# Kernel optimization log

Measured on AMD Instinct MI355X. Metric: run time of the kernel, lower is better.

The kernel has to match this reference:

```python
import jax, jax.numpy as jnp
import numpy as np

N = 64        # n_nodes per graph
H = 128       # hidden channels (128x0e + 128x1o)
NB = 8        # radial bessel basis size
L = 2         # num_interactions
R_MAX = 5.0
AVG_NEIGH = 63.0
DIM = 3       # output vector dim
B = 64        # batch (vmapped)
T = 32        # time-embedding dim
S = 5         # num_species


def _edges(n):
    # fully-connected graph, no self loops (static shapes, jit-friendly)
    s, r = np.meshgrid(np.arange(n), np.arange(n), indexing='ij')
    m = s != r
    return jnp.asarray(s[m]), jnp.asarray(r[m])


def setup_inputs() -> dict:
    key = jax.random.key(0)
    ks = jax.random.split(key, 12)
    sc = 0.05
    return {
        'positions': jax.random.normal(ks[0], (B, N, 3), jnp.float32),
        'node_features': jax.random.randint(ks[1], (B, N), 0, S).astype(jnp.int64),
        'global_features': jax.random.normal(ks[2], (B, T), jnp.float32),
        'emb': jax.random.normal(ks[3], (S, H), jnp.float32) * sc,
        'Wt': jax.random.normal(ks[4], (T, H), jnp.float32) * sc,
        'Wr1': jax.random.normal(ks[5], (L, NB, H), jnp.float32) * sc,
        'Wr2': jax.random.normal(ks[6], (L, H, H), jnp.float32) * sc,
        'Wupd': jax.random.normal(ks[7], (L, H, H), jnp.float32) * sc,
        'Wmix': jax.random.normal(ks[8], (L, H, H), jnp.float32) * sc,
        'Wg1': jax.random.normal(ks[9], (H, H), jnp.float32) * sc,
        'Wg2': jax.random.normal(ks[10], (H, H), jnp.float32) * sc,
        'final_scaling': jnp.ones((), jnp.float32),
    }


def _call_single(pos, z, t, emb, Wt, Wr1, Wr2, Wupd, Wmix, Wg1, Wg2, final_scaling):
    snd, rcv = _edges(N)
    ev = pos[rcv] - pos[snd]                               # [E,3] edge vectors (gather)
    r = jnp.sqrt(jnp.sum(ev * ev, axis=-1) + 1e-12)        # [E]
    u = ev / r[:, None]                                    # unit directions
    # Bessel radial basis with cosine cutoff (r_max acts as soft radius graph)
    n = jnp.arange(1, NB + 1, dtype=pos.dtype)
    rb = jnp.sin(n * jnp.pi * r[:, None] / R_MAX) / r[:, None]   # [E,NB]
    fc = 0.5 * (jnp.cos(jnp.pi * r / R_MAX) + 1.0) * (r < R_MAX)
    rb = rb * fc[:, None]
    # node embedding from species + time embedding
    h = emb[z] + t @ Wt                                    # [N,H] scalar features
    v = jnp.zeros((N, H, DIM), pos.dtype)                  # vector (1o) features
    for l in range(L):
        w = jax.nn.silu(rb @ Wr1[l]) @ Wr2[l]              # [E,H] radial weights
        m0 = w * h[snd]                                    # [E,H] scalar messages
        m1 = m0[:, :, None] * u[:, None, :]                # [E,H,3] vector messages
        a0 = jax.ops.segment_sum(m0, rcv, num_segments=N) / AVG_NEIGH
        a1 = jax.ops.segment_sum(m1, rcv, num_segments=N) / AVG_NEIGH
        h = h + a0 @ Wupd[l]
        v = v + jnp.einsum('ngd,gh->nhd', a1, Wmix[l])
    # equivariant readout: scalar gate per channel contracts vector channels
    g = jax.nn.silu(h @ Wg1) @ Wg2                         # [N,H]
    out = jnp.einsum('nhd,nh->nd', v, g)                   # [N,3]
    return out * final_scaling


def reference(positions, node_features, global_features, emb, Wt, Wr1, Wr2, Wupd, Wmix, Wg1, Wg2, final_scaling):
    f = lambda p, z, t: _call_single(p, z, t, emb, Wt, Wr1, Wr2, Wupd, Wmix, Wg1, Wg2, final_scaling)
    return jax.vmap(f)(positions, node_features, global_features)
```

## Files before the change

### kernel.cpp

```cpp
#include <hip/hip_runtime.h>
#include <math.h>

#define NN 64
#define HH 128
#define NBB 8
#define TT 32
#define BB 64
#define NROW (BB * NN)
#define PLANE ((size_t)NROW * HH)
#define WR1OFF (8 * 16384)

typedef __attribute__((ext_vector_type(8))) short short8;
typedef __attribute__((ext_vector_type(4))) float f32x4;
typedef __attribute__((ext_vector_type(2))) float f32x2;
typedef __attribute__((ext_vector_type(2))) unsigned int u32x2;

__device__ __forceinline__ float silu_f(float x) {
  return x * __builtin_amdgcn_rcpf(1.0f + __expf(-x));
}

__device__ __forceinline__ unsigned short bf1(float x) {
  __bf16 h = (__bf16)x;
  return *(unsigned short*)&h;
}
__device__ __forceinline__ unsigned bf2(float lo, float hi) {
  return (unsigned)bf1(lo) | ((unsigned)bf1(hi) << 16);
}

__device__ __forceinline__ void gemm8(
    const unsigned short (*sA)[136], const unsigned short* __restrict__ Bp,
    int w, int nlo, int quad, f32x4 C[2]) {
  const short8 z8 = {0, 0, 0, 0, 0, 0, 0, 0};
  short8 afr[4];
#pragma unroll
  for (int kt = 0; kt < 4; ++kt)
    afr[kt] = (nlo < 8) ? *(const short8*)&sA[nlo][kt * 32 + quad * 8] : z8;
#pragma unroll
  for (int nt = 0; nt < 2; ++nt)
#pragma unroll
    for (int kt = 0; kt < 4; ++kt) {
      short8 bfr = *(const short8*)&Bp[((kt * 128 + w * 32 + nt * 16 + nlo) * 4 + quad) * 8];
      C[nt] = __builtin_amdgcn_mfma_f32_16x16x32_bf16(afr[kt], bfr, C[nt], 0, 0, 0);
    }
}

__global__ __launch_bounds__(256) void k_init(
    const float* __restrict__ emb, const int* __restrict__ z,
    const float* __restrict__ gf, const float* __restrict__ Wt,
    const float* __restrict__ Wr1, const float* __restrict__ Wr2,
    const float* __restrict__ Wupd, const float* __restrict__ Wmix,
    const float* __restrict__ Wg1, const float* __restrict__ Wg2,
    float* __restrict__ h, unsigned short* __restrict__ Wpack) {
  __shared__ float tvec[HH];
  __shared__ int sz[NN];
  int b4 = blockIdx.x, tid = threadIdx.x;
#pragma unroll
  for (int ii = 0; ii < 2; ++ii) {
    int idx = b4 * 512 + ii * 256 + tid;
    int m = idx >> 14;
    int local = idx & 16383;
    float val;
    if (m < 2) val = Wr2[idx];
    else if (m < 4) val = Wupd[idx - 32768];
    else if (m < 6) val = Wmix[idx - 65536];
    else if (m == 6) val = Wg1[local];
    else val = Wg2[local];
    int k = local >> 7, n = local & 127;
    int kt = k >> 5, q = (k >> 3) & 3, j = k & 7;
    Wpack[(idx & ~16383) + (((kt * 128 + n) * 4 + q) * 8) + j] = bf1(val);
  }
  if (tid < 32) {
    int e = b4 * 32 + tid;
    int l = e >> 12, p = e & 4095;
    int n = p >> 5, q = (p >> 3) & 3, j = p & 7;
    float val = (q == 0) ? Wr1[l * NBB * HH + j * HH + n] : 0.f;
    Wpack[WR1OFF + l * 4096 + p] = bf1(val);
  }
  if (b4 < 64) {
    int b = b4;
    if (tid < NN) sz[tid] = z[b * NN + tid];
    if (tid < HH) {
      float acc = 0.f;
#pragma unroll
      for (int k = 0; k < TT; ++k) acc += gf[b * TT + k] * Wt[k * HH + tid];
      tvec[tid] = acc;
    }
    __syncthreads();
    for (int i = tid; i < NN * HH; i += 256) {
      int n = i >> 7, c = i & 127;
      h[(size_t)b * NN * HH + i] = emb[sz[n] * HH + c] + tvec[c];
    }
  }
}

__global__ __launch_bounds__(256) void k_layer(
    const float* __restrict__ pos,
    const float* __restrict__ hA,
    const unsigned short* __restrict__ a0in,
    unsigned short* __restrict__ apout,
    const unsigned short* __restrict__ Wpack,
    int l) {
  __shared__ __align__(16) unsigned short sh_S[NN][136];
  __shared__ __align__(16) unsigned short sh_M0T[4][32][72];
  __shared__ __align__(16) unsigned short sh_rbh[2][NN][8];
  __shared__ __align__(16) unsigned short sh_ub[2][4][NN];

  int blk = blockIdx.x;
  int b = blk >> 5, rp = blk & 31;
  int r0 = rp * 2;
  int tid = threadIdx.x;
  int w = tid >> 6, lane = tid & 63;
  int nlo = lane & 15, quad = lane >> 4;

  f32x4 hbv[4][2];
#pragma unroll
  for (int mt = 0; mt < 4; ++mt)
#pragma unroll
    for (int nt = 0; nt < 2; ++nt)
#pragma unroll
      for (int reg = 0; reg < 4; ++reg)
        hbv[mt][nt][reg] =
            hA[((size_t)b * NN + mt * 16 + quad * 4 + reg) * HH + w * 32 + nt * 16 + nlo];

  {
    int s = tid & 63;
    int ksel = (tid >> 6) & 1;
    int ri = (tid >> 7) & 1;
    int r = r0 + ri;
    const float* pb = pos + b * NN * 3;
    float dx = pb[r * 3 + 0] - pb[s * 3 + 0];
    float dy = pb[r * 3 + 1] - pb[s * 3 + 1];
    float dz = pb[r * 3 + 2] - pb[s * 3 + 2];
    float rr = sqrtf(dx * dx + dy * dy + dz * dz + 1e-12f);
    float inv = __builtin_amdgcn_rcpf(rr);
    const float invAvg = 1.0f / 63.0f;
    if (ksel == 0) {
      float ia = inv * invAvg;
      sh_ub[ri][1][s] = bf1(dx * ia);
      sh_ub[ri][2][s] = bf1(dy * ia);
      sh_ub[ri][3][s] = bf1(dz * ia);
    } else {
      sh_ub[ri][0][s] = bf1(invAvg);
    }
    const float PI_OVER_5 = 0.628318530717958647692f;
    float fc = (s != r && rr < 5.0f) ? 0.5f * (__cosf(PI_OVER_5 * rr) + 1.0f) : 0.0f;
    float base = PI_OVER_5 * rr;
    float sc = inv * fc;
    int k0 = ksel * 4;
    float v0 = __sinf((float)(k0 + 1) * base) * sc;
    float v1 = __sinf((float)(k0 + 2) * base) * sc;
    float v2 = __sinf((float)(k0 + 3) * base) * sc;
    float v3 = __sinf((float)(k0 + 4) * base) * sc;
    *(unsigned*)&sh_rbh[ri][s][k0]     = bf2(v0, v1);
    *(unsigned*)&sh_rbh[ri][s][k0 + 2] = bf2(v2, v3);
  }
  if (l) {
    for (int i = tid; i < NN * 64; i += 256) {
      int s = i >> 6, c2 = (i & 63) * 2;
      *(unsigned*)&sh_S[s][c2] =
          *(const unsigned*)&a0in[((size_t)b * NN + s) * HH + c2];
    }
  }
  __syncthreads();

  if (l) {
    const unsigned short* Bu = Wpack + 2 * 16384;
#pragma unroll
    for (int mt = 0; mt < 4; ++mt) {
      short8 afr[4];
#pragma unroll
      for (int kt = 0; kt < 4; ++kt)
        afr[kt] = *(const short8*)&sh_S[mt * 16 + nlo][kt * 32 + quad * 8];
#pragma unroll
      for (int nt = 0; nt < 2; ++nt)
#pragma unroll
        for (int kt = 0; kt < 4; ++kt) {
          short8 bfr = *(const short8*)&Bu[((kt * 128 + w * 32 + nt * 16 + nlo) * 4 + quad) * 8];
          hbv[mt][nt] = __builtin_amdgcn_mfma_f32_16x16x32_bf16(afr[kt], bfr, hbv[mt][nt], 0, 0, 0);
        }
    }
    __syncthreads();
  }

  const unsigned short* Wr1p = Wpack + WR1OFF + l * 4096;
  short8 bw[2];
#pragma unroll
  for (int nt = 0; nt < 2; ++nt)
    bw[nt] = *(const short8*)&Wr1p[((w * 32 + nt * 16 + nlo) * 4 + quad) * 8];
  const unsigned short* Bbase = Wpack + l * 16384;
  short8 bfr[4][2];
#pragma unroll
  for (int kt = 0; kt < 4; ++kt)
#pragma unroll
    for (int nt = 0; nt < 2; ++nt)
      bfr[kt][nt] = *(const short8*)&Bbase[((kt * 128 + w * 32 + nt * 16 + nlo) * 4 + quad) * 8];

  const short8 zero8 = {0, 0, 0, 0, 0, 0, 0, 0};
  short8 au[2][2];
#pragma unroll
  for (int ri = 0; ri < 2; ++ri)
#pragma unroll
    for (int kt = 0; kt < 2; ++kt)
      au[ri][kt] = (nlo < 4) ? *(const short8*)&sh_ub[ri][nlo][kt * 32 + quad * 8] : zero8;

#pragma unroll
  for (int ri = 0; ri < 2; ++ri) {
#pragma unroll
    for (int mtp = 0; mtp < 2; ++mtp) {
      f32x4 Cs[2][2];
#pragma unroll
      for (int mi = 0; mi < 2; ++mi)
#pragma unroll
        for (int nt = 0; nt < 2; ++nt) Cs[mi][nt] = (f32x4){0.f, 0.f, 0.f, 0.f};
#pragma unroll
      for (int mi = 0; mi < 2; ++mi) {
        int mt = mtp * 2 + mi;
        short8 afr = (quad == 0) ? *(const short8*)&sh_rbh[ri][mt * 16 + nlo][0] : zero8;
#pragma unroll
        for (int nt = 0; nt < 2; ++nt)
          Cs[mi][nt] = __builtin_amdgcn_mfma_f32_16x16x32_bf16(afr, bw[nt], Cs[mi][nt], 0, 0, 0);
      }
#pragma unroll
      for (int mi = 0; mi < 2; ++mi)
#pragma unroll
        for (int nt = 0; nt < 2; ++nt)
#pragma unroll
          for (int reg = 0; reg < 4; ++reg) {
            int s = (mtp * 2 + mi) * 16 + quad * 4 + reg;
            int c = w * 32 + nt * 16 + nlo;
            sh_S[s][c] = bf1(silu_f(Cs[mi][nt][reg]));
          }
    }
    __syncthreads();

#pragma unroll
    for (int mt = 0; mt < 4; ++mt) {
      short8 afr[4];
      int s_a = mt * 16 + nlo;
#pragma unroll
      for (int kt = 0; kt < 4; ++kt)
        afr[kt] = *(const short8*)&sh_S[s_a][kt * 32 + quad * 8];
#pragma unroll
      for (int nt = 0; nt < 2; ++nt) {
        f32x4 C = {0.f, 0.f, 0.f, 0.f};
#pragma unroll
        for (int kt = 0; kt < 4; ++kt)
          C = __builtin_amdgcn_mfma_f32_16x16x32_bf16(afr[kt], bfr[kt][nt], C, 0, 0, 0);
        f32x4 m0 = C * hbv[mt][nt];
        u32x2 pk;
        pk.x = bf2(m0[0], m0[1]);
        pk.y = bf2(m0[2], m0[3]);
        *(u32x2*)&sh_M0T[w][nt * 16 + nlo][mt * 16 + quad * 4] = pk;
      }
    }
    {
      f32x4 Cu[2] = {{0, 0, 0, 0}, {0, 0, 0, 0}};
#pragma unroll
      for (int nt = 0; nt < 2; ++nt)
#pragma unroll
        for (int kt = 0; kt < 2; ++kt) {
          short8 bm = *(const short8*)&sh_M0T[w][nt * 16 + nlo][kt * 32 + quad * 8];
          Cu[nt] = __builtin_amdgcn_mfma_f32_16x16x32_bf16(au[ri][kt], bm, Cu[nt], 0, 0, 0);
        }
      if (quad == 0) {
#pragma unroll
        for (int nt = 0; nt < 2; ++nt) {
          size_t base = (size_t)(b * NN + r0 + ri) * HH + w * 32 + nt * 16 + nlo;
#pragma unroll
          for (int reg = 0; reg < 4; ++reg)
            apout[(l * 4 + reg) * PLANE + base] = bf1(Cu[nt][reg]);
        }
      }
    }
    if (ri == 0) __syncthreads();
  }
}

__global__ __launch_bounds__(256) void k_update_ro(
    const unsigned short* __restrict__ apbf, const float* __restrict__ hA,
    const unsigned short* __restrict__ Wpack,
    const float* __restrict__ fs, float* __restrict__ out) {
  __shared__ __align__(16) unsigned short sh_a[8][8][136];
  __shared__ __align__(16) unsigned short sh_h[8][136];
  __shared__ float red[4][8][3];
  int tid = threadIdx.x, w = tid >> 6, lane = tid & 63;
  int nlo = lane & 15, quad = lane >> 4;
  int row0 = blockIdx.x * 8;
  for (int i = tid; i < 8 * 8 * 64; i += 256) {
    int p = i >> 9, rr = (i >> 6) & 7, c2 = (i & 63) * 2;
    *(unsigned*)&sh_a[p][rr][c2] =
        *(const unsigned*)&apbf[p * PLANE + (size_t)(row0 + rr) * HH + c2];
  }
  f32x4 Ch[2];
#pragma unroll
  for (int nt = 0; nt < 2; ++nt)
#pragma unroll
    for (int reg = 0; reg < 4; ++reg)
      Ch[nt][reg] = (quad < 2)
          ? hA[(size_t)(row0 + quad * 4 + reg) * HH + w * 32 + nt * 16 + nlo] : 0.f;
  __syncthreads();
  gemm8(sh_a[0], Wpack + 2 * 16384, w, nlo, quad, Ch);
  gemm8(sh_a[4], Wpack + 3 * 16384, w, nlo, quad, Ch);
  f32x4 Cx[2] = {{0,0,0,0},{0,0,0,0}};
  f32x4 Cy[2] = {{0,0,0,0},{0,0,0,0}};
  f32x4 Cz[2] = {{0,0,0,0},{0,0,0,0}};
  gemm8(sh_a[1], Wpack + 4 * 16384, w, nlo, quad, Cx);
  gemm8(sh_a[5], Wpack + 5 * 16384, w, nlo, quad, Cx);
  gemm8(sh_a[2], Wpack + 4 * 16384, w, nlo, quad, Cy);
  gemm8(sh_a[6], Wpack + 5 * 16384, w, nlo, quad, Cy);
  gemm8(sh_a[3], Wpack + 4 * 16384, w, nlo, quad, Cz);
  gemm8(sh_a[7], Wpack + 5 * 16384, w, nlo, quad, Cz);
  if (quad < 2) {
#pragma unroll
    for (int nt = 0; nt < 2; ++nt)
#pragma unroll
      for (int reg = 0; reg < 4; ++reg)
        sh_h[quad * 4 + reg][w * 32 + nt * 16 + nlo] = bf1(Ch[nt][reg]);
  }
  __syncthreads();
  unsigned short (*sh_q)[136] = sh_a[0];
  f32x4 Cq[2] = {{0,0,0,0},{0,0,0,0}};
  gemm8(sh_h, Wpack + 6 * 16384, w, nlo, quad, Cq);
  if (quad < 2) {
#pragma unroll
    for (int nt = 0; nt < 2; ++nt)
#pragma unroll
      for (int reg = 0; reg < 4; ++reg)
        sh_q[quad * 4 + reg][w * 32 + nt * 16 + nlo] = bf1(silu_f(Cq[nt][reg]));
  }
  __syncthreads();
  f32x4 Cg[2] = {{0,0,0,0},{0,0,0,0}};
  gemm8(sh_q, Wpack + 7 * 16384, w, nlo, quad, Cg);
  float pr[3][4];
#pragma unroll
  for (int d = 0; d < 3; ++d)
#pragma unroll
    for (int reg = 0; reg < 4; ++reg) pr[d][reg] = 0.f;
#pragma unroll
  for (int nt = 0; nt < 2; ++nt)
#pragma unroll
    for (int reg = 0; reg < 4; ++reg) {
      float gv = Cg[nt][reg];
      pr[0][reg] += gv * Cx[nt][reg];
      pr[1][reg] += gv * Cy[nt][reg];
      pr[2][reg] += gv * Cz[nt][reg];
    }
#pragma unroll
  for (int off = 1; off < 16; off <<= 1)
#pragma unroll
    for (int d = 0; d < 3; ++d)
#pragma unroll
      for (int reg = 0; reg < 4; ++reg)
        pr[d][reg] += __shfl_xor(pr[d][reg], off);
  if (nlo == 0 && quad < 2) {
#pragma unroll
    for (int d = 0; d < 3; ++d)
#pragma unroll
      for (int reg = 0; reg < 4; ++reg)
        red[w][quad * 4 + reg][d] = pr[d][reg];
  }
  __syncthreads();
  if (tid < 24) {
    int row = tid / 3, d = tid % 3;
    float s = red[0][row][d] + red[1][row][d] + red[2][row][d] + red[3][row][d];
    out[(size_t)(row0 + row) * 3 + d] = s * fs[0];
  }
}

extern "C" void kernel_launch(void* const* d_in, const int* in_sizes, int n_in,
                              void* d_out, int out_size, void* d_ws, size_t ws_size,
                              hipStream_t stream) {
  const float* pos  = (const float*)d_in[0];
  const int*   z    = (const int*)d_in[1];
  const float* gf   = (const float*)d_in[2];
  const float* emb  = (const float*)d_in[3];
  const float* Wt   = (const float*)d_in[4];
  const float* Wr1  = (const float*)d_in[5];
  const float* Wr2  = (const float*)d_in[6];
  const float* Wupd = (const float*)d_in[7];
  const float* Wmix = (const float*)d_in[8];
  const float* Wg1  = (const float*)d_in[9];
  const float* Wg2  = (const float*)d_in[10];
  const float* fs   = (const float*)d_in[11];
  float* out = (float*)d_out;

  float* ws = (float*)d_ws;
  float* hA = ws;
  unsigned short* apbf = (unsigned short*)(ws + PLANE);
  unsigned short* Wpack = (unsigned short*)(ws + 5 * PLANE);

  k_init<<<dim3(256), dim3(256), 0, stream>>>(emb, z, gf, Wt, Wr1, Wr2, Wupd,
                                              Wmix, Wg1, Wg2, hA, Wpack);
  k_layer<<<dim3(BB * 32), dim3(256), 0, stream>>>(pos, hA, apbf, apbf, Wpack, 0);
  k_layer<<<dim3(BB * 32), dim3(256), 0, stream>>>(pos, hA, apbf, apbf, Wpack, 1);
  k_update_ro<<<dim3(512), dim3(256), 0, stream>>>(apbf, hA, Wpack, fs, out);
}
```

Before: 153.1 us.

## Process four receivers per layer block and vectorize weight packing writes

Each k_layer block now handles four receiver nodes in two passes of two instead of two. The grid is halved, so the per-block setup (loading hA into registers, loading packed weights, and the layer-1 update GEMM that recomputes h) is amortized over twice as many receivers. The weight-pack loop in k_init now computes two consecutive k values per thread and writes them as one 32-bit store, with reads strided by k. Fewer blocks (1024) could reduce latency hiding and adds an extra sequential pass inside each block.

```diff
diff --git a/kernel.cpp b/kernel.cpp
--- a/kernel.cpp
+++ b/kernel.cpp
@@ -54,20 +54,25 @@
   __shared__ float tvec[HH];
   __shared__ int sz[NN];
   int b4 = blockIdx.x, tid = threadIdx.x;
-#pragma unroll
-  for (int ii = 0; ii < 2; ++ii) {
-    int idx = b4 * 512 + ii * 256 + tid;
-    int m = idx >> 14;
-    int local = idx & 16383;
-    float val;
-    if (m < 2) val = Wr2[idx];
-    else if (m < 4) val = Wupd[idx - 32768];
-    else if (m < 6) val = Wmix[idx - 65536];
-    else if (m == 6) val = Wg1[local];
-    else val = Wg2[local];
-    int k = local >> 7, n = local & 127;
-    int kt = k >> 5, q = (k >> 3) & 3, j = k & 7;
-    Wpack[(idx & ~16383) + (((kt * 128 + n) * 4 + q) * 8) + j] = bf1(val);
+  {
+    int p2 = b4 * 256 + tid;
+    int p = p2 * 2;
+    int m = p >> 14;
+    int j = p & 7;
+    int q = (p >> 3) & 3;
+    int n = (p >> 5) & 127;
+    int kt = (p >> 12) & 3;
+    int k = kt * 32 + q * 8 + j;
+    const float* src;
+    int base;
+    if (m < 2) { src = Wr2; base = m * 16384; }
+    else if (m < 4) { src = Wupd; base = (m - 2) * 16384; }
+    else if (m < 6) { src = Wmix; base = (m - 4) * 16384; }
+    else if (m == 6) { src = Wg1; base = 0; }
+    else { src = Wg2; base = 0; }
+    float v0 = src[base + k * 128 + n];
+    float v1 = src[base + (k + 1) * 128 + n];
+    *(unsigned*)&Wpack[p] = bf2(v0, v1);
   }
   if (tid < 32) {
     int e = b4 * 32 + tid;
@@ -106,8 +111,8 @@
   __shared__ __align__(16) unsigned short sh_ub[2][4][NN];
 
   int blk = blockIdx.x;
-  int b = blk >> 5, rp = blk & 31;
-  int r0 = rp * 2;
+  int b = blk >> 4, rp4 = blk & 15;
+  int r0 = rp4 * 4;
   int tid = threadIdx.x;
   int w = tid >> 6, lane = tid & 63;
   int nlo = lane & 15, quad = lane >> 4;
@@ -121,66 +126,6 @@
       for (int reg = 0; reg < 4; ++reg)
         hbv[mt][nt][reg] =
             hA[((size_t)b * NN + mt * 16 + quad * 4 + reg) * HH + w * 32 + nt * 16 + nlo];
-
-  {
-    int s = tid & 63;
-    int ksel = (tid >> 6) & 1;
-    int ri = (tid >> 7) & 1;
-    int r = r0 + ri;
-    const float* pb = pos + b * NN * 3;
-    float dx = pb[r * 3 + 0] - pb[s * 3 + 0];
-    float dy = pb[r * 3 + 1] - pb[s * 3 + 1];
-    float dz = pb[r * 3 + 2] - pb[s * 3 + 2];
-    float rr = sqrtf(dx * dx + dy * dy + dz * dz + 1e-12f);
-    float inv = __builtin_amdgcn_rcpf(rr);
-    const float invAvg = 1.0f / 63.0f;
-    if (ksel == 0) {
-      float ia = inv * invAvg;
-      sh_ub[ri][1][s] = bf1(dx * ia);
-      sh_ub[ri][2][s] = bf1(dy * ia);
-      sh_ub[ri][3][s] = bf1(dz * ia);
-    } else {
-      sh_ub[ri][0][s] = bf1(invAvg);
-    }
-    const float PI_OVER_5 = 0.628318530717958647692f;
-    float fc = (s != r && rr < 5.0f) ? 0.5f * (__cosf(PI_OVER_5 * rr) + 1.0f) : 0.0f;
-    float base = PI_OVER_5 * rr;
-    float sc = inv * fc;
-    int k0 = ksel * 4;
-    float v0 = __sinf((float)(k0 + 1) * base) * sc;
-    float v1 = __sinf((float)(k0 + 2) * base) * sc;
-    float v2 = __sinf((float)(k0 + 3) * base) * sc;
-    float v3 = __sinf((float)(k0 + 4) * base) * sc;
-    *(unsigned*)&sh_rbh[ri][s][k0]     = bf2(v0, v1);
-    *(unsigned*)&sh_rbh[ri][s][k0 + 2] = bf2(v2, v3);
-  }
-  if (l) {
-    for (int i = tid; i < NN * 64; i += 256) {
-      int s = i >> 6, c2 = (i & 63) * 2;
-      *(unsigned*)&sh_S[s][c2] =
-          *(const unsigned*)&a0in[((size_t)b * NN + s) * HH + c2];
-    }
-  }
-  __syncthreads();
-
-  if (l) {
-    const unsigned short* Bu = Wpack + 2 * 16384;
-#pragma unroll
-    for (int mt = 0; mt < 4; ++mt) {
-      short8 afr[4];
-#pragma unroll
-      for (int kt = 0; kt < 4; ++kt)
-        afr[kt] = *(const short8*)&sh_S[mt * 16 + nlo][kt * 32 + quad * 8];
-#pragma unroll
-      for (int nt = 0; nt < 2; ++nt)
-#pragma unroll
-        for (int kt = 0; kt < 4; ++kt) {
-          short8 bfr = *(const short8*)&Bu[((kt * 128 + w * 32 + nt * 16 + nlo) * 4 + quad) * 8];
-          hbv[mt][nt] = __builtin_amdgcn_mfma_f32_16x16x32_bf16(afr[kt], bfr, hbv[mt][nt], 0, 0, 0);
-        }
-    }
-    __syncthreads();
-  }
 
   const unsigned short* Wr1p = Wpack + WR1OFF + l * 4096;
   short8 bw[2];
@@ -196,83 +141,149 @@
       bfr[kt][nt] = *(const short8*)&Bbase[((kt * 128 + w * 32 + nt * 16 + nlo) * 4 + quad) * 8];
 
   const short8 zero8 = {0, 0, 0, 0, 0, 0, 0, 0};
-  short8 au[2][2];
-#pragma unroll
-  for (int ri = 0; ri < 2; ++ri)
-#pragma unroll
-    for (int kt = 0; kt < 2; ++kt)
-      au[ri][kt] = (nlo < 4) ? *(const short8*)&sh_ub[ri][nlo][kt * 32 + quad * 8] : zero8;
-
-#pragma unroll
-  for (int ri = 0; ri < 2; ++ri) {
-#pragma unroll
-    for (int mtp = 0; mtp < 2; ++mtp) {
-      f32x4 Cs[2][2];
-#pragma unroll
-      for (int mi = 0; mi < 2; ++mi)
-#pragma unroll
-        for (int nt = 0; nt < 2; ++nt) Cs[mi][nt] = (f32x4){0.f, 0.f, 0.f, 0.f};
-#pragma unroll
-      for (int mi = 0; mi < 2; ++mi) {
-        int mt = mtp * 2 + mi;
-        short8 afr = (quad == 0) ? *(const short8*)&sh_rbh[ri][mt * 16 + nlo][0] : zero8;
+
+#pragma unroll
+  for (int pp = 0; pp < 2; ++pp) {
+    int rb0 = r0 + pp * 2;
+
+    {
+      int s = tid & 63;
+      int ksel = (tid >> 6) & 1;
+      int ri = (tid >> 7) & 1;
+      int r = rb0 + ri;
+      const float* pb = pos + b * NN * 3;
+      float dx = pb[r * 3 + 0] - pb[s * 3 + 0];
+      float dy = pb[r * 3 + 1] - pb[s * 3 + 1];
+      float dz = pb[r * 3 + 2] - pb[s * 3 + 2];
+      float rr = sqrtf(dx * dx + dy * dy + dz * dz + 1e-12f);
+      float inv = __builtin_amdgcn_rcpf(rr);
+      const float invAvg = 1.0f / 63.0f;
+      if (ksel == 0) {
+        float ia = inv * invAvg;
+        sh_ub[ri][1][s] = bf1(dx * ia);
+        sh_ub[ri][2][s] = bf1(dy * ia);
+        sh_ub[ri][3][s] = bf1(dz * ia);
+      } else {
+        sh_ub[ri][0][s] = bf1(invAvg);
+      }
+      const float PI_OVER_5 = 0.628318530717958647692f;
+      float fc = (s != r && rr < 5.0f) ? 0.5f * (__cosf(PI_OVER_5 * rr) + 1.0f) : 0.0f;
+      float base = PI_OVER_5 * rr;
+      float sc = inv * fc;
+      int k0 = ksel * 4;
+      float v0 = __sinf((float)(k0 + 1) * base) * sc;
+      float v1 = __sinf((float)(k0 + 2) * base) * sc;
+      float v2 = __sinf((float)(k0 + 3) * base) * sc;
+      float v3 = __sinf((float)(k0 + 4) * base) * sc;
+      *(unsigned*)&sh_rbh[ri][s][k0]     = bf2(v0, v1);
+      *(unsigned*)&sh_rbh[ri][s][k0 + 2] = bf2(v2, v3);
+    }
+    if (pp == 0 && l) {
+      for (int i = tid; i < NN * 64; i += 256) {
+        int s = i >> 6, c2 = (i & 63) * 2;
+        *(unsigned*)&sh_S[s][c2] =
+            *(const unsigned*)&a0in[((size_t)b * NN + s) * HH + c2];
+      }
+    }
+    __syncthreads();
+
+    if (pp == 0 && l) {
+      const unsigned short* Bu = Wpack + 2 * 16384;
+#pragma unroll
+      for (int mt = 0; mt < 4; ++mt) {
+        short8 afr[4];
+#pragma unroll
+        for (int kt = 0; kt < 4; ++kt)
+          afr[kt] = *(const short8*)&sh_S[mt * 16 + nlo][kt * 32 + quad * 8];
 #pragma unroll
         for (int nt = 0; nt < 2; ++nt)
-          Cs[mi][nt] = __builtin_amdgcn_mfma_f32_16x16x32_bf16(afr, bw[nt], Cs[mi][nt], 0, 0, 0);
-      }
-#pragma unroll
-      for (int mi = 0; mi < 2; ++mi)
+#pragma unroll
+          for (int kt = 0; kt < 4; ++kt) {
+            short8 bfr2 = *(const short8*)&Bu[((kt * 128 + w * 32 + nt * 16 + nlo) * 4 + quad) * 8];
+            hbv[mt][nt] = __builtin_amdgcn_mfma_f32_16x16x32_bf16(afr[kt], bfr2, hbv[mt][nt], 0, 0, 0);
+          }
+      }
+      __syncthreads();
+    }
+
+    short8 au[2][2];
+#pragma unroll
+    for (int ri = 0; ri < 2; ++ri)
+#pragma unroll
+      for (int kt = 0; kt < 2; ++kt)
+        au[ri][kt] = (nlo < 4) ? *(const short8*)&sh_ub[ri][nlo][kt * 32 + quad * 8] : zero8;
+
+#pragma unroll
+    for (int ri = 0; ri < 2; ++ri) {
+#pragma unroll
+      for (int mtp = 0; mtp < 2; ++mtp) {
+        f32x4 Cs[2][2];
+#pragma unroll
+        for (int mi = 0; mi < 2; ++mi)
+#pragma unroll
+          for (int nt = 0; nt < 2; ++nt) Cs[mi][nt] = (f32x4){0.f, 0.f, 0.f, 0.f};
+#pragma unroll
+        for (int mi = 0; mi < 2; ++mi) {
+          int mt = mtp * 2 + mi;
+          short8 afr = (quad == 0) ? *(const short8*)&sh_rbh[ri][mt * 16 + nlo][0] : zero8;
+#pragma unroll
+          for (int nt = 0; nt < 2; ++nt)
+            Cs[mi][nt] = __builtin_amdgcn_mfma_f32_16x16x32_bf16(afr, bw[nt], Cs[mi][nt], 0, 0, 0);
+        }
+#pragma unroll
+        for (int mi = 0; mi < 2; ++mi)
+#pragma unroll
+          for (int nt = 0; nt < 2; ++nt)
+#pragma unroll
+            for (int reg = 0; reg < 4; ++reg) {
+              int s = (mtp * 2 + mi) * 16 + quad * 4 + reg;
+              int c = w * 32 + nt * 16 + nlo;
+              sh_S[s][c] = bf1(silu_f(Cs[mi][nt][reg]));
+            }
+      }
+      __syncthreads();
+
+#pragma unroll
+      for (int mt = 0; mt < 4; ++mt) {
+        short8 afr[4];
+        int s_a = mt * 16 + nlo;
+#pragma unroll
+        for (int kt = 0; kt < 4; ++kt)
+          afr[kt] = *(const short8*)&sh_S[s_a][kt * 32 + quad * 8];
+#pragma unroll
+        for (int nt = 0; nt < 2; ++nt) {
+          f32x4 C = {0.f, 0.f, 0.f, 0.f};
+#pragma unroll
+          for (int kt = 0; kt < 4; ++kt)
+            C = __builtin_amdgcn_mfma_f32_16x16x32_bf16(afr[kt], bfr[kt][nt], C, 0, 0, 0);
+          f32x4 m0 = C * hbv[mt][nt];
+          u32x2 pk;
+          pk.x = bf2(m0[0], m0[1]);
+          pk.y = bf2(m0[2], m0[3]);
+          *(u32x2*)&sh_M0T[w][nt * 16 + nlo][mt * 16 + quad * 4] = pk;
+        }
+      }
+      {
+        f32x4 Cu[2] = {{0, 0, 0, 0}, {0, 0, 0, 0}};
 #pragma unroll
         for (int nt = 0; nt < 2; ++nt)
 #pragma unroll
-          for (int reg = 0; reg < 4; ++reg) {
-            int s = (mtp * 2 + mi) * 16 + quad * 4 + reg;
-            int c = w * 32 + nt * 16 + nlo;
-            sh_S[s][c] = bf1(silu_f(Cs[mi][nt][reg]));
+          for (int kt = 0; kt < 2; ++kt) {
+            short8 bm = *(const short8*)&sh_M0T[w][nt * 16 + nlo][kt * 32 + quad * 8];
+            Cu[nt] = __builtin_amdgcn_mfma_f32_16x16x32_bf16(au[ri][kt], bm, Cu[nt], 0, 0, 0);
           }
-    }
-    __syncthreads();
-
-#pragma unroll
-    for (int mt = 0; mt < 4; ++mt) {
-      short8 afr[4];
-      int s_a = mt * 16 + nlo;
-#pragma unroll
-      for (int kt = 0; kt < 4; ++kt)
-        afr[kt] = *(const short8*)&sh_S[s_a][kt * 32 + quad * 8];
-#pragma unroll
-      for (int nt = 0; nt < 2; ++nt) {
-        f32x4 C = {0.f, 0.f, 0.f, 0.f};
-#pragma unroll
-        for (int kt = 0; kt < 4; ++kt)
-          C = __builtin_amdgcn_mfma_f32_16x16x32_bf16(afr[kt], bfr[kt][nt], C, 0, 0, 0);
-        f32x4 m0 = C * hbv[mt][nt];
-        u32x2 pk;
-        pk.x = bf2(m0[0], m0[1]);
-        pk.y = bf2(m0[2], m0[3]);
-        *(u32x2*)&sh_M0T[w][nt * 16 + nlo][mt * 16 + quad * 4] = pk;
-      }
-    }
-    {
-      f32x4 Cu[2] = {{0, 0, 0, 0}, {0, 0, 0, 0}};
-#pragma unroll
-      for (int nt = 0; nt < 2; ++nt)
-#pragma unroll
-        for (int kt = 0; kt < 2; ++kt) {
-          short8 bm = *(const short8*)&sh_M0T[w][nt * 16 + nlo][kt * 32 + quad * 8];
-          Cu[nt] = __builtin_amdgcn_mfma_f32_16x16x32_bf16(au[ri][kt], bm, Cu[nt], 0, 0, 0);
+        if (quad == 0) {
+#pragma unroll
+          for (int nt = 0; nt < 2; ++nt) {
+            size_t base = (size_t)(b * NN + rb0 + ri) * HH + w * 32 + nt * 16 + nlo;
+#pragma unroll
+            for (int reg = 0; reg < 4; ++reg)
+              apout[(l * 4 + reg) * PLANE + base] = bf1(Cu[nt][reg]);
+          }
         }
-      if (quad == 0) {
-#pragma unroll
-        for (int nt = 0; nt < 2; ++nt) {
-          size_t base = (size_t)(b * NN + r0 + ri) * HH + w * 32 + nt * 16 + nlo;
-#pragma unroll
-          for (int reg = 0; reg < 4; ++reg)
-            apout[(l * 4 + reg) * PLANE + base] = bf1(Cu[nt][reg]);
-        }
-      }
-    }
-    if (ri == 0) __syncthreads();
+      }
+      if (!(pp == 1 && ri == 1)) __syncthreads();
+    }
   }
 }
 
@@ -391,7 +402,7 @@
 
   k_init<<<dim3(256), dim3(256), 0, stream>>>(emb, z, gf, Wt, Wr1, Wr2, Wupd,
                                               Wmix, Wg1, Wg2, hA, Wpack);
-  k_layer<<<dim3(BB * 32), dim3(256), 0, stream>>>(pos, hA, apbf, apbf, Wpack, 0);
-  k_layer<<<dim3(BB * 32), dim3(256), 0, stream>>>(pos, hA, apbf, apbf, Wpack, 1);
+  k_layer<<<dim3(BB * 16), dim3(256), 0, stream>>>(pos, hA, apbf, apbf, Wpack, 0);
+  k_layer<<<dim3(BB * 16), dim3(256), 0, stream>>>(pos, hA, apbf, apbf, Wpack, 1);
   k_update_ro<<<dim3(512), dim3(256), 0, stream>>>(apbf, hA, Wpack, fs, out);
 }
```

New measurement: 146.3 us. 4.4% less time.
